# Kernel optimization log

Hardware: AMD Instinct MI355X
Metric: run time of the kernel (lower is better)

The kernel has to match this reference:

```python
import jax, jax.numpy as jnp
import numpy as np


def setup_inputs() -> dict:
    key = jax.random.key(0)
    ks = jax.random.split(key, 6)
    B, S, H, I, E = 2, 1024, 1024, 2816, 8
    W = 0.02  # weight init scale
    return {
        "x": jax.random.normal(ks[0], (B, S, H), jnp.float32),
        "w_router": jax.random.normal(ks[1], (H, E), jnp.float32) * W,
        "w_gate": jax.random.normal(ks[2], (E, H, I), jnp.float32) * W,
        "w_up": jax.random.normal(ks[3], (E, H, I), jnp.float32) * W,
        "w_down": jax.random.normal(ks[4], (E, I, H), jnp.float32) * W,
        "b_down": jnp.zeros((E, H), jnp.float32),
    }


def reference(x, w_router, w_gate, w_up, w_down, b_down):
    # Eval path of PrunedLlamaSMoEBlock: noiseless router, top-k select, softmax
    # over selected logits, SwiGLU experts, scatter-add combine.
    NUM_SELECTS = 2
    T = x.shape[0] * x.shape[1]
    E = w_router.shape[1]
    flat_x = x.reshape(T, -1)                      # [T,H]

    logits = flat_x @ w_router                     # [T,E]
    top_vals, top_idx = jax.lax.top_k(logits, NUM_SELECTS)   # [T,k]
    gw = jax.nn.softmax(top_vals.astype(jnp.float32), axis=1).astype(x.dtype)

    # Dense combine weights: combine[t,e] = sum_k gw[t,k] * (top_idx[t,k]==e)
    combine = jnp.zeros((T, E), x.dtype).at[
        jnp.arange(T)[:, None], top_idx
    ].add(gw)                                      # [T,E]

    # SwiGLU experts over all tokens (weighted by combine, zero if unselected)
    g = jnp.einsum("th,ehi->tei", flat_x, w_gate)  # [T,E,I]
    u = jnp.einsum("th,ehi->tei", flat_x, w_up)    # [T,E,I]
    a = jax.nn.silu(g) * u                         # [T,E,I]
    y = jnp.einsum("tei,eih->teh", a, w_down) + b_down[None]  # [T,E,H]

    out = jnp.einsum("te,teh->th", combine, y)     # [T,H]
    return out.reshape(x.shape)
```

## Files before the change

### kernel.cpp

```cpp
#include <hip/hip_runtime.h>
#include <math.h>

#define HD __device__ __forceinline__

constexpr int TT = 2048;
constexpr int HH = 1024;
constexpr int II = 2816;
constexpr int EE = 8;
constexpr int NK1 = HH / 64;
constexpr int NK2 = II / 64;
constexpr int KS2 = 2;
constexpr int HALF2 = NK2 / KS2;
constexpr int MAXTILES = 40;

typedef short  bf16x8  __attribute__((ext_vector_type(8)));
typedef float  floatx4 __attribute__((ext_vector_type(4)));
typedef unsigned short ushortx8 __attribute__((ext_vector_type(8)));

constexpr size_t OFF_XB    = 0;
constexpr size_t OFF_WGT   = OFF_XB    + (size_t)TT*HH*2;
constexpr size_t OFF_WUT   = OFF_WGT   + (size_t)EE*II*HH*2;
constexpr size_t OFF_WDT   = OFF_WUT   + (size_t)EE*II*HH*2;
constexpr size_t OFF_ABUF  = OFF_WDT   + (size_t)EE*HH*II*2;
constexpr size_t OFF_CNT   = OFF_ABUF  + (size_t)2*TT*II*2;
constexpr size_t OFF_OFFS  = OFF_CNT   + 256;
constexpr size_t OFF_MDESC = OFF_OFFS  + 256;
constexpr size_t OFF_EMETA = OFF_MDESC + 256;
constexpr size_t OFF_WMETA = OFF_EMETA + 16384;
constexpr size_t OFF_TLIST = OFF_WMETA + 16384;
constexpr size_t OFF_GWL   = OFF_TLIST + 16384;

HD unsigned short f2bf(float f) {
  union { float f; unsigned int u; } v; v.f = f;
  return (unsigned short)((v.u + 0x7fffu + ((v.u >> 16) & 1u)) >> 16);
}

HD void load_lds16(const void* gptr, void* lptr) {
  __builtin_amdgcn_global_load_lds(
      (const __attribute__((address_space(1))) void*)gptr,
      (__attribute__((address_space(3))) void*)lptr,
      16, 0, 0);
}

__global__ __launch_bounds__(256)
void prep_kernel(const float* __restrict__ x, unsigned short* __restrict__ xb,
                 float* __restrict__ out, int* __restrict__ counts) {
  const int i = blockIdx.x * blockDim.x + threadIdx.x;
  if (i < EE) counts[i] = 0;
  const float4 z = {0.f, 0.f, 0.f, 0.f};
  ((float4*)out)[i] = z;
  float4 v = ((const float4*)x)[i];
  ushort4 o;
  o.x = f2bf(v.x); o.y = f2bf(v.y); o.z = f2bf(v.z); o.w = f2bf(v.w);
  ((ushort4*)xb)[i] = o;
}

__global__ __launch_bounds__(256)
void transpose_cast_kernel(const float* __restrict__ wg, const float* __restrict__ wu,
                           const float* __restrict__ wd,
                           unsigned short* __restrict__ wgt, unsigned short* __restrict__ wut,
                           unsigned short* __restrict__ wdt) {
  const int e = blockIdx.y / 3;
  const int t = blockIdx.y % 3;
  const float* src; unsigned short* dst; int R, C;
  if (t == 0)      { src = wg; dst = wgt; R = HH; C = II; }
  else if (t == 1) { src = wu; dst = wut; R = HH; C = II; }
  else             { src = wd; dst = wdt; R = II; C = HH; }
  const int nct = C / 128;
  const int rt = blockIdx.x / nct;
  const int ct = blockIdx.x % nct;
  const size_t base = (size_t)e * R * C;
  const int R0 = rt * 64;
  const int C0 = ct * 128;

  const int lane = threadIdx.x & 63;
  const int wave = threadIdx.x >> 6;
  const int r0 = R0 + (lane & 7) * 8;
  const int c0 = C0 + wave * 32 + (lane >> 3) * 4;

  floatx4 v[8];
  const float* sp = src + base + (size_t)r0 * C + c0;
#pragma unroll
  for (int j = 0; j < 8; ++j)
    v[j] = __builtin_nontemporal_load((const floatx4*)(sp + (size_t)j * C));

  unsigned short* dp = dst + base + (size_t)c0 * R + r0;
#pragma unroll
  for (int jj = 0; jj < 4; ++jj) {
    ushortx8 o;
#pragma unroll
    for (int j = 0; j < 8; ++j) o[j] = f2bf(v[j][jj]);
    *(ushortx8*)(dp + (size_t)jj * R) = o;
  }
}

__global__ __launch_bounds__(64)
void router_kernel(const float* __restrict__ x, const float* __restrict__ w_router,
                   int* __restrict__ counts, int* __restrict__ emeta, float* __restrict__ wmeta) {
  const int t = blockIdx.x;
  const int lane = threadIdx.x;
  float acc[EE];
#pragma unroll
  for (int e = 0; e < EE; ++e) acc[e] = 0.f;
  for (int h = lane; h < HH; h += 64) {
    const float xv = x[(size_t)t * HH + h];
    const float* wr = w_router + (size_t)h * EE;
#pragma unroll
    for (int e = 0; e < EE; ++e) acc[e] += xv * wr[e];
  }
#pragma unroll
  for (int e = 0; e < EE; ++e) {
#pragma unroll
    for (int off = 32; off > 0; off >>= 1) acc[e] += __shfl_xor(acc[e], off, 64);
  }
  if (lane == 0) {
    int e0 = 0; float v0 = acc[0];
#pragma unroll
    for (int e = 1; e < EE; ++e) if (acc[e] > v0) { v0 = acc[e]; e0 = e; }
    int e1 = -1; float v1 = -3.4e38f;
#pragma unroll
    for (int e = 0; e < EE; ++e) if (e != e0 && acc[e] > v1) { v1 = acc[e]; e1 = e; }
    const float ex = __expf(v1 - v0);
    const float s  = 1.f + ex;
    emeta[2 * t] = e0; emeta[2 * t + 1] = e1;
    wmeta[2 * t] = 1.f / s; wmeta[2 * t + 1] = ex / s;
    atomicAdd(&counts[e0], 1);
    atomicAdd(&counts[e1], 1);
  }
}

__global__ __launch_bounds__(256)
void scanfill_kernel(const int* __restrict__ counts, const int* __restrict__ emeta,
                     const float* __restrict__ wmeta,
                     int* __restrict__ offsets, int* __restrict__ mdesc,
                     int* __restrict__ token_list, float* __restrict__ gw_list) {
  __shared__ int s_off[EE];
  __shared__ int s_fill[EE];
  const int tid = threadIdx.x;
  if (tid < EE) s_fill[tid] = 0;
  if (tid == 0) {
    int s = 0;
    int nt = 0;
    for (int e = 0; e < EE; ++e) {
      const int c = counts[e];
      s_off[e] = s; offsets[e] = s;
      for (int m = 0; m < c; m += 128) mdesc[1 + nt++] = (e << 20) | m;
      s += c;
    }
    offsets[EE] = s;
    mdesc[0] = nt;
  }
  __syncthreads();
  for (int t = tid; t < TT; t += 256) {
#pragma unroll
    for (int s = 0; s < 2; ++s) {
      const int e = emeta[2 * t + s];
      const int pos = atomicAdd(&s_fill[e], 1);
      token_list[s_off[e] + pos] = t;
      gw_list[s_off[e] + pos] = wmeta[2 * t + s];
    }
  }
}

__global__ __launch_bounds__(256, 4)
void gemm1_kernel(const unsigned short* __restrict__ xb,
                  const unsigned short* __restrict__ wgt,
                  const unsigned short* __restrict__ wut,
                  const int* __restrict__ offsets,
                  const int* __restrict__ mdesc,
                  const int* __restrict__ token_list,
                  unsigned short* __restrict__ Abuf) {
  if ((int)blockIdx.y >= mdesc[0]) return;
  const int d = mdesc[1 + blockIdx.y];
  const int e = d >> 20;
  const int m_base = d & 0xFFFFF;
  const int off_e = offsets[e];
  const int n_e = offsets[e + 1] - off_e;
  const int n_base = blockIdx.x * 64;

  __shared__ __attribute__((aligned(16))) unsigned short ldsA[128 * 64];
  __shared__ __attribute__((aligned(16))) unsigned short ldsG[64 * 64];
  __shared__ __attribute__((aligned(16))) unsigned short ldsU[64 * 64];

  const int tid = threadIdx.x;
  const int wave = tid >> 6;
  const int lane = tid & 63;
  const int quad = lane >> 4;
  const int l16 = lane & 15;
  const int wave_m = (wave & 1) * 64;
  const int wave_n = (wave >> 1) * 32;

  const int srow = lane >> 3;
  const int clog = (lane & 7) ^ srow;

  const unsigned short* gA[4];
  const unsigned short* gG[2];
  const unsigned short* gU[2];
#pragma unroll
  for (int it = 0; it < 4; ++it) {
    const int r = it * 32 + wave * 8 + srow;
    int ar = m_base + r; if (ar > n_e - 1) ar = n_e - 1;
    const int tok = token_list[off_e + ar];
    gA[it] = xb + (size_t)tok * HH + clog * 8;
  }
#pragma unroll
  for (int it = 0; it < 2; ++it) {
    const int r = it * 32 + wave * 8 + srow;
    gG[it] = wgt + ((size_t)e * II + (n_base + r)) * HH + clog * 8;
    gU[it] = wut + ((size_t)e * II + (n_base + r)) * HH + clog * 8;
  }

  floatx4 accG[4][2], accU[4][2];
  const floatx4 fz = {0.f, 0.f, 0.f, 0.f};
#pragma unroll
  for (int i = 0; i < 4; ++i)
#pragma unroll
    for (int j = 0; j < 2; ++j) { accG[i][j] = fz; accU[i][j] = fz; }

  for (int kt = 0; kt < NK1; ++kt) {
    const int k0 = kt * 64;
#pragma unroll
    for (int it = 0; it < 4; ++it)
      load_lds16(gA[it] + k0, &ldsA[(it * 32 + wave * 8) * 64]);
#pragma unroll
    for (int it = 0; it < 2; ++it) {
      load_lds16(gG[it] + k0, &ldsG[(it * 32 + wave * 8) * 64]);
      load_lds16(gU[it] + k0, &ldsU[(it * 32 + wave * 8) * 64]);
    }
    __syncthreads();
#pragma unroll
    for (int ks = 0; ks < 2; ++ks) {
      bf16x8 af[4], bg[2], bu[2];
#pragma unroll
      for (int f = 0; f < 4; ++f) {
        const int rowA = wave_m + f * 16 + l16;
        const int cA = (ks * 4 + quad) ^ (rowA & 7);
        af[f] = *(const bf16x8*)&ldsA[rowA * 64 + cA * 8];
      }
#pragma unroll
      for (int f = 0; f < 2; ++f) {
        const int rowB = wave_n + f * 16 + l16;
        const int cB = (ks * 4 + quad) ^ (rowB & 7);
        bg[f] = *(const bf16x8*)&ldsG[rowB * 64 + cB * 8];
        bu[f] = *(const bf16x8*)&ldsU[rowB * 64 + cB * 8];
      }
#pragma unroll
      for (int mf = 0; mf < 4; ++mf)
#pragma unroll
        for (int nf = 0; nf < 2; ++nf) {
          accG[mf][nf] = __builtin_amdgcn_mfma_f32_16x16x32_bf16(af[mf], bg[nf], accG[mf][nf], 0, 0, 0);
          accU[mf][nf] = __builtin_amdgcn_mfma_f32_16x16x32_bf16(af[mf], bu[nf], accU[mf][nf], 0, 0, 0);
        }
    }
    __syncthreads();
  }

#pragma unroll
  for (int mf = 0; mf < 4; ++mf)
#pragma unroll
    for (int nf = 0; nf < 2; ++nf) {
      const int col = n_base + wave_n + nf * 16 + l16;
#pragma unroll
      for (int j = 0; j < 4; ++j) {
        const int r = m_base + wave_m + mf * 16 + quad * 4 + j;
        if (r < n_e) {
          const float g = accG[mf][nf][j];
          const float u = accU[mf][nf][j];
          const float a = (g / (1.f + __expf(-g))) * u;
          Abuf[(size_t)(off_e + r) * II + col] = f2bf(a);
        }
      }
    }
}

__global__ __launch_bounds__(256, 4)
void gemm2_kernel(const unsigned short* __restrict__ Abuf,
                  const unsigned short* __restrict__ wdt,
                  const float* __restrict__ b_down,
                  const int* __restrict__ offsets,
                  const int* __restrict__ mdesc,
                  const int* __restrict__ token_list,
                  const float* __restrict__ gw_list,
                  float* __restrict__ out) {
  if ((int)blockIdx.y >= mdesc[0]) return;
  const int d = mdesc[1 + blockIdx.y];
  const int e = d >> 20;
  const int m_base = d & 0xFFFFF;
  const int off_e = offsets[e];
  const int n_e = offsets[e + 1] - off_e;
  const int n_base = blockIdx.x * 64;
  const int split = blockIdx.z;
  const int kt_lo = split * HALF2;
  const int kt_hi = kt_lo + HALF2;

  __shared__ __attribute__((aligned(16))) unsigned short ldsA[128 * 64];
  __shared__ __attribute__((aligned(16))) unsigned short ldsB[64 * 64];

  const int tid = threadIdx.x;
  const int wave = tid >> 6;
  const int lane = tid & 63;
  const int quad = lane >> 4;
  const int l16 = lane & 15;
  const int wave_m = (wave & 1) * 64;
  const int wave_n = (wave >> 1) * 32;

  const int srow = lane >> 3;
  const int clog = (lane & 7) ^ srow;

  const unsigned short* gA[4];
  const unsigned short* gB[2];
#pragma unroll
  for (int it = 0; it < 4; ++it) {
    const int r = it * 32 + wave * 8 + srow;
    int ar = m_base + r; if (ar > n_e - 1) ar = n_e - 1;
    gA[it] = Abuf + (size_t)(off_e + ar) * II + clog * 8;
  }
#pragma unroll
  for (int it = 0; it < 2; ++it) {
    const int r = it * 32 + wave * 8 + srow;
    gB[it] = wdt + ((size_t)e * HH + (n_base + r)) * II + clog * 8;
  }

  floatx4 acc[4][2];
  const floatx4 fz = {0.f, 0.f, 0.f, 0.f};
#pragma unroll
  for (int i = 0; i < 4; ++i)
#pragma unroll
    for (int j = 0; j < 2; ++j) acc[i][j] = fz;

  for (int kt = kt_lo; kt < kt_hi; ++kt) {
    const int k0 = kt * 64;
#pragma unroll
    for (int it = 0; it < 4; ++it)
      load_lds16(gA[it] + k0, &ldsA[(it * 32 + wave * 8) * 64]);
#pragma unroll
    for (int it = 0; it < 2; ++it)
      load_lds16(gB[it] + k0, &ldsB[(it * 32 + wave * 8) * 64]);
    __syncthreads();
#pragma unroll
    for (int ks = 0; ks < 2; ++ks) {
      bf16x8 af[4], bf[2];
#pragma unroll
      for (int f = 0; f < 4; ++f) {
        const int rowA = wave_m + f * 16 + l16;
        const int cA = (ks * 4 + quad) ^ (rowA & 7);
        af[f] = *(const bf16x8*)&ldsA[rowA * 64 + cA * 8];
      }
#pragma unroll
      for (int f = 0; f < 2; ++f) {
        const int rowB = wave_n + f * 16 + l16;
        const int cB = (ks * 4 + quad) ^ (rowB & 7);
        bf[f] = *(const bf16x8*)&ldsB[rowB * 64 + cB * 8];
      }
#pragma unroll
      for (int mf = 0; mf < 4; ++mf)
#pragma unroll
        for (int nf = 0; nf < 2; ++nf)
          acc[mf][nf] = __builtin_amdgcn_mfma_f32_16x16x32_bf16(af[mf], bf[nf], acc[mf][nf], 0, 0, 0);
    }
    __syncthreads();
  }

#pragma unroll
  for (int mf = 0; mf < 4; ++mf)
#pragma unroll
    for (int nf = 0; nf < 2; ++nf) {
      const int col = n_base + wave_n + nf * 16 + l16;
      const float bd = (split == 0) ? b_down[e * HH + col] : 0.f;
#pragma unroll
      for (int j = 0; j < 4; ++j) {
        const int r = m_base + wave_m + mf * 16 + quad * 4 + j;
        if (r < n_e) {
          const int cr = off_e + r;
          const int tok = token_list[cr];
          const float gw = gw_list[cr];
          atomicAdd(&out[(size_t)tok * HH + col], gw * (acc[mf][nf][j] + bd));
        }
      }
    }
}

extern "C" void kernel_launch(void* const* d_in, const int* in_sizes, int n_in,
                              void* d_out, int out_size, void* d_ws, size_t ws_size,
                              hipStream_t stream) {
  const float* x        = (const float*)d_in[0];
  const float* w_router = (const float*)d_in[1];
  const float* w_gate   = (const float*)d_in[2];
  const float* w_up     = (const float*)d_in[3];
  const float* w_down   = (const float*)d_in[4];
  const float* b_down   = (const float*)d_in[5];
  float* out = (float*)d_out;

  char* ws = (char*)d_ws;
  unsigned short* xb   = (unsigned short*)(ws + OFF_XB);
  unsigned short* wgt  = (unsigned short*)(ws + OFF_WGT);
  unsigned short* wut  = (unsigned short*)(ws + OFF_WUT);
  unsigned short* wdt  = (unsigned short*)(ws + OFF_WDT);
  unsigned short* Abuf = (unsigned short*)(ws + OFF_ABUF);
  int*   counts  = (int*)(ws + OFF_CNT);
  int*   offsets = (int*)(ws + OFF_OFFS);
  int*   mdesc   = (int*)(ws + OFF_MDESC);
  int*   emeta   = (int*)(ws + OFF_EMETA);
  float* wmeta   = (float*)(ws + OFF_WMETA);
  int*   tlist   = (int*)(ws + OFF_TLIST);
  float* gwl     = (float*)(ws + OFF_GWL);

  prep_kernel<<<TT * HH / 4 / 256, 256, 0, stream>>>(x, xb, out, counts);
  router_kernel<<<TT, 64, 0, stream>>>(x, w_router, counts, emeta, wmeta);
  scanfill_kernel<<<1, 256, 0, stream>>>(counts, emeta, wmeta, offsets, mdesc, tlist, gwl);
  transpose_cast_kernel<<<dim3(352, 3 * EE), 256, 0, stream>>>(
      w_gate, w_up, w_down, wgt, wut, wdt);
  gemm1_kernel<<<dim3(II / 64, MAXTILES), 256, 0, stream>>>(xb, wgt, wut, offsets, mdesc, tlist, Abuf);
  gemm2_kernel<<<dim3(HH / 64, MAXTILES, KS2), 256, 0, stream>>>(Abuf, wdt, b_down, offsets, mdesc, tlist, gwl, out);
}
```

Before: 450.1 us.

## Replace gemm2 atomic scatter with slot buffer and a separate combine kernel

gemm2 now writes per-slot fp32 partial results for each K-split into a buffer instead of atomically adding weighted results into the output. A new combine kernel gathers each token's two expert slots and both splits, adds the bias, applies the gate weights and writes the output once, so the output no longer needs zeroing. The scanfill step is parallelised per expert with a prefix scan that builds a token-to-slot map. The gemm2 tile grows to 128 columns with launch bounds lowered to 3 blocks. The aim is to remove global atomic contention, at the cost of an extra kernel and extra fp32 buffer traffic that reuses the gate/up weight workspace.

```diff
diff --git a/kernel.cpp b/kernel.cpp
--- a/kernel.cpp
+++ b/kernel.cpp
@@ -12,6 +12,7 @@
 constexpr int KS2 = 2;
 constexpr int HALF2 = NK2 / KS2;
 constexpr int MAXTILES = 40;
+constexpr int NSLOT = 2 * TT;
 
 typedef short  bf16x8  __attribute__((ext_vector_type(8)));
 typedef float  floatx4 __attribute__((ext_vector_type(4)));
@@ -28,7 +29,8 @@
 constexpr size_t OFF_EMETA = OFF_MDESC + 256;
 constexpr size_t OFF_WMETA = OFF_EMETA + 16384;
 constexpr size_t OFF_TLIST = OFF_WMETA + 16384;
-constexpr size_t OFF_GWL   = OFF_TLIST + 16384;
+constexpr size_t OFF_SLOT  = OFF_TLIST + 16384;
+constexpr size_t OFF_YBUF  = OFF_WGT;
 
 HD unsigned short f2bf(float f) {
   union { float f; unsigned int u; } v; v.f = f;
@@ -44,11 +46,9 @@
 
 __global__ __launch_bounds__(256)
 void prep_kernel(const float* __restrict__ x, unsigned short* __restrict__ xb,
-                 float* __restrict__ out, int* __restrict__ counts) {
+                 int* __restrict__ counts) {
   const int i = blockIdx.x * blockDim.x + threadIdx.x;
   if (i < EE) counts[i] = 0;
-  const float4 z = {0.f, 0.f, 0.f, 0.f};
-  ((float4*)out)[i] = z;
   float4 v = ((const float4*)x)[i];
   ushort4 o;
   o.x = f2bf(v.x); o.y = f2bf(v.y); o.z = f2bf(v.z); o.w = f2bf(v.w);
@@ -131,33 +131,53 @@
 
 __global__ __launch_bounds__(256)
 void scanfill_kernel(const int* __restrict__ counts, const int* __restrict__ emeta,
-                     const float* __restrict__ wmeta,
                      int* __restrict__ offsets, int* __restrict__ mdesc,
-                     int* __restrict__ token_list, float* __restrict__ gw_list) {
-  __shared__ int s_off[EE];
-  __shared__ int s_fill[EE];
+                     int* __restrict__ token_list, int* __restrict__ slotmap) {
+  const int e = blockIdx.x;
   const int tid = threadIdx.x;
-  if (tid < EE) s_fill[tid] = 0;
-  if (tid == 0) {
-    int s = 0;
-    int nt = 0;
-    for (int e = 0; e < EE; ++e) {
-      const int c = counts[e];
-      s_off[e] = s; offsets[e] = s;
-      for (int m = 0; m < c; m += 128) mdesc[1 + nt++] = (e << 20) | m;
+  int off_e = 0;
+#pragma unroll
+  for (int i = 0; i < EE; ++i) { const int c = counts[i]; if (i < e) off_e += c; }
+  if (e == 0 && tid == 0) {
+    int s = 0, nt = 0;
+    for (int i = 0; i < EE; ++i) {
+      const int c = counts[i];
+      offsets[i] = s;
+      for (int m = 0; m < c; m += 128) mdesc[1 + nt++] = (i << 20) | m;
       s += c;
     }
     offsets[EE] = s;
     mdesc[0] = nt;
   }
+  constexpr int CH = TT / 256;
+  const int t0 = tid * CH;
+  int cnt = 0;
+  for (int k = 0; k < CH; ++k) {
+    const int t = t0 + k;
+    if (emeta[2 * t] == e) ++cnt;
+    if (emeta[2 * t + 1] == e) ++cnt;
+  }
+  __shared__ int s_scan[256];
+  s_scan[tid] = cnt;
   __syncthreads();
-  for (int t = tid; t < TT; t += 256) {
+  int v = cnt;
+  for (int d = 1; d < 256; d <<= 1) {
+    const int add = (tid >= d) ? s_scan[tid - d] : 0;
+    __syncthreads();
+    v += add;
+    s_scan[tid] = v;
+    __syncthreads();
+  }
+  int pos = off_e + (v - cnt);
+  for (int k = 0; k < CH; ++k) {
+    const int t = t0 + k;
 #pragma unroll
     for (int s = 0; s < 2; ++s) {
-      const int e = emeta[2 * t + s];
-      const int pos = atomicAdd(&s_fill[e], 1);
-      token_list[s_off[e] + pos] = t;
-      gw_list[s_off[e] + pos] = wmeta[2 * t + s];
+      if (emeta[2 * t + s] == e) {
+        token_list[pos] = t;
+        slotmap[2 * t + s] = pos;
+        ++pos;
+      }
     }
   }
 }
@@ -273,28 +293,25 @@
     }
 }
 
-__global__ __launch_bounds__(256, 4)
+__global__ __launch_bounds__(256, 3)
 void gemm2_kernel(const unsigned short* __restrict__ Abuf,
                   const unsigned short* __restrict__ wdt,
-                  const float* __restrict__ b_down,
                   const int* __restrict__ offsets,
                   const int* __restrict__ mdesc,
-                  const int* __restrict__ token_list,
-                  const float* __restrict__ gw_list,
-                  float* __restrict__ out) {
+                  float* __restrict__ Ybuf) {
   if ((int)blockIdx.y >= mdesc[0]) return;
   const int d = mdesc[1 + blockIdx.y];
   const int e = d >> 20;
   const int m_base = d & 0xFFFFF;
   const int off_e = offsets[e];
   const int n_e = offsets[e + 1] - off_e;
-  const int n_base = blockIdx.x * 64;
+  const int n_base = blockIdx.x * 128;
   const int split = blockIdx.z;
   const int kt_lo = split * HALF2;
   const int kt_hi = kt_lo + HALF2;
 
   __shared__ __attribute__((aligned(16))) unsigned short ldsA[128 * 64];
-  __shared__ __attribute__((aligned(16))) unsigned short ldsB[64 * 64];
+  __shared__ __attribute__((aligned(16))) unsigned short ldsB[128 * 64];
 
   const int tid = threadIdx.x;
   const int wave = tid >> 6;
@@ -302,13 +319,13 @@
   const int quad = lane >> 4;
   const int l16 = lane & 15;
   const int wave_m = (wave & 1) * 64;
-  const int wave_n = (wave >> 1) * 32;
+  const int wave_n = (wave >> 1) * 64;
 
   const int srow = lane >> 3;
   const int clog = (lane & 7) ^ srow;
 
   const unsigned short* gA[4];
-  const unsigned short* gB[2];
+  const unsigned short* gB[4];
 #pragma unroll
   for (int it = 0; it < 4; ++it) {
     const int r = it * 32 + wave * 8 + srow;
@@ -316,17 +333,17 @@
     gA[it] = Abuf + (size_t)(off_e + ar) * II + clog * 8;
   }
 #pragma unroll
-  for (int it = 0; it < 2; ++it) {
+  for (int it = 0; it < 4; ++it) {
     const int r = it * 32 + wave * 8 + srow;
     gB[it] = wdt + ((size_t)e * HH + (n_base + r)) * II + clog * 8;
   }
 
-  floatx4 acc[4][2];
+  floatx4 acc[4][4];
   const floatx4 fz = {0.f, 0.f, 0.f, 0.f};
 #pragma unroll
   for (int i = 0; i < 4; ++i)
 #pragma unroll
-    for (int j = 0; j < 2; ++j) acc[i][j] = fz;
+    for (int j = 0; j < 4; ++j) acc[i][j] = fz;
 
   for (int kt = kt_lo; kt < kt_hi; ++kt) {
     const int k0 = kt * 64;
@@ -334,12 +351,12 @@
     for (int it = 0; it < 4; ++it)
       load_lds16(gA[it] + k0, &ldsA[(it * 32 + wave * 8) * 64]);
 #pragma unroll
-    for (int it = 0; it < 2; ++it)
+    for (int it = 0; it < 4; ++it)
       load_lds16(gB[it] + k0, &ldsB[(it * 32 + wave * 8) * 64]);
     __syncthreads();
 #pragma unroll
     for (int ks = 0; ks < 2; ++ks) {
-      bf16x8 af[4], bf[2];
+      bf16x8 af[4], bf[4];
 #pragma unroll
       for (int f = 0; f < 4; ++f) {
         const int rowA = wave_m + f * 16 + l16;
@@ -347,7 +364,7 @@
         af[f] = *(const bf16x8*)&ldsA[rowA * 64 + cA * 8];
       }
 #pragma unroll
-      for (int f = 0; f < 2; ++f) {
+      for (int f = 0; f < 4; ++f) {
         const int rowB = wave_n + f * 16 + l16;
         const int cB = (ks * 4 + quad) ^ (rowB & 7);
         bf[f] = *(const bf16x8*)&ldsB[rowB * 64 + cB * 8];
@@ -355,29 +372,48 @@
 #pragma unroll
       for (int mf = 0; mf < 4; ++mf)
 #pragma unroll
-        for (int nf = 0; nf < 2; ++nf)
+        for (int nf = 0; nf < 4; ++nf)
           acc[mf][nf] = __builtin_amdgcn_mfma_f32_16x16x32_bf16(af[mf], bf[nf], acc[mf][nf], 0, 0, 0);
     }
     __syncthreads();
   }
 
+  float* yb = Ybuf + (size_t)split * NSLOT * HH;
 #pragma unroll
   for (int mf = 0; mf < 4; ++mf)
 #pragma unroll
-    for (int nf = 0; nf < 2; ++nf) {
+    for (int nf = 0; nf < 4; ++nf) {
       const int col = n_base + wave_n + nf * 16 + l16;
-      const float bd = (split == 0) ? b_down[e * HH + col] : 0.f;
 #pragma unroll
       for (int j = 0; j < 4; ++j) {
         const int r = m_base + wave_m + mf * 16 + quad * 4 + j;
-        if (r < n_e) {
-          const int cr = off_e + r;
-          const int tok = token_list[cr];
-          const float gw = gw_list[cr];
-          atomicAdd(&out[(size_t)tok * HH + col], gw * (acc[mf][nf][j] + bd));
-        }
-      }
-    }
+        if (r < n_e)
+          yb[(size_t)(off_e + r) * HH + col] = acc[mf][nf][j];
+      }
+    }
+}
+
+__global__ __launch_bounds__(256)
+void combine_kernel(const float* __restrict__ Ybuf, const int* __restrict__ slotmap,
+                    const int* __restrict__ emeta, const float* __restrict__ wmeta,
+                    const float* __restrict__ b_down, float* __restrict__ out) {
+  const int t = blockIdx.x;
+  const int c = threadIdx.x;
+  const int s0 = slotmap[2 * t], s1 = slotmap[2 * t + 1];
+  const int e0 = emeta[2 * t], e1 = emeta[2 * t + 1];
+  const float g0 = wmeta[2 * t], g1 = wmeta[2 * t + 1];
+  const float4 y00 = ((const float4*)(Ybuf + (size_t)s0 * HH))[c];
+  const float4 y01 = ((const float4*)(Ybuf + ((size_t)NSLOT + s0) * HH))[c];
+  const float4 y10 = ((const float4*)(Ybuf + (size_t)s1 * HH))[c];
+  const float4 y11 = ((const float4*)(Ybuf + ((size_t)NSLOT + s1) * HH))[c];
+  const float4 b0 = ((const float4*)(b_down + (size_t)e0 * HH))[c];
+  const float4 b1 = ((const float4*)(b_down + (size_t)e1 * HH))[c];
+  float4 o;
+  o.x = g0 * (y00.x + y01.x + b0.x) + g1 * (y10.x + y11.x + b1.x);
+  o.y = g0 * (y00.y + y01.y + b0.y) + g1 * (y10.y + y11.y + b1.y);
+  o.z = g0 * (y00.z + y01.z + b0.z) + g1 * (y10.z + y11.z + b1.z);
+  o.w = g0 * (y00.w + y01.w + b0.w) + g1 * (y10.w + y11.w + b1.w);
+  ((float4*)(out + (size_t)t * HH))[c] = o;
 }
 
 extern "C" void kernel_launch(void* const* d_in, const int* in_sizes, int n_in,
@@ -403,13 +439,15 @@
   int*   emeta   = (int*)(ws + OFF_EMETA);
   float* wmeta   = (float*)(ws + OFF_WMETA);
   int*   tlist   = (int*)(ws + OFF_TLIST);
-  float* gwl     = (float*)(ws + OFF_GWL);
-
-  prep_kernel<<<TT * HH / 4 / 256, 256, 0, stream>>>(x, xb, out, counts);
+  int*   slotmap = (int*)(ws + OFF_SLOT);
+  float* Ybuf    = (float*)(ws + OFF_YBUF);
+
+  prep_kernel<<<TT * HH / 4 / 256, 256, 0, stream>>>(x, xb, counts);
   router_kernel<<<TT, 64, 0, stream>>>(x, w_router, counts, emeta, wmeta);
-  scanfill_kernel<<<1, 256, 0, stream>>>(counts, emeta, wmeta, offsets, mdesc, tlist, gwl);
+  scanfill_kernel<<<EE, 256, 0, stream>>>(counts, emeta, offsets, mdesc, tlist, slotmap);
   transpose_cast_kernel<<<dim3(352, 3 * EE), 256, 0, stream>>>(
       w_gate, w_up, w_down, wgt, wut, wdt);
   gemm1_kernel<<<dim3(II / 64, MAXTILES), 256, 0, stream>>>(xb, wgt, wut, offsets, mdesc, tlist, Abuf);
-  gemm2_kernel<<<dim3(HH / 64, MAXTILES, KS2), 256, 0, stream>>>(Abuf, wdt, b_down, offsets, mdesc, tlist, gwl, out);
-}
+  gemm2_kernel<<<dim3(HH / 128, MAXTILES, KS2), 256, 0, stream>>>(Abuf, wdt, offsets, mdesc, Ybuf);
+  combine_kernel<<<TT, 256, 0, stream>>>(Ybuf, slotmap, emeta, wmeta, b_down, out);
+}
```

Measured after the change: 431.8 us. 1.04x faster.
